# Kernel optimization log

Hardware: AMD Instinct MI355X
Metric: run time of the kernel (lower is better)

Reference implementation:

```python
import jax, jax.numpy as jnp
import numpy as np

# Domain bounds and training nu-range (from init_kwargs)
X_MIN, X_MAX = -1.0, 1.0
Y_MIN, Y_MAX = -1.0, 1.0
T_MIN, T_MAX = 0.0, 1.0
NU_MIN, NU_MAX = 0.01, 0.1

LAYERS = [4, 256, 256, 256, 256, 2]
N = 16384  # collocation points


def setup_inputs() -> dict:
    key = jax.random.key(0)
    ks = jax.random.split(key, 4 + 2 * (len(LAYERS) - 1))
    inp = {
        'x': jax.random.uniform(ks[0], (N, 1), minval=X_MIN, maxval=X_MAX, dtype=jnp.float32),
        'y': jax.random.uniform(ks[1], (N, 1), minval=Y_MIN, maxval=Y_MAX, dtype=jnp.float32),
        't': jax.random.uniform(ks[2], (N, 1), minval=T_MIN, maxval=T_MAX, dtype=jnp.float32),
        'nu': jax.random.uniform(ks[3], (N, 1), minval=NU_MIN, maxval=NU_MAX, dtype=jnp.float32),
    }
    # glorot_normal weights, zero biases (keras Dense defaults)
    for i in range(len(LAYERS) - 1):
        fan_in, fan_out = LAYERS[i], LAYERS[i + 1]
        std = (2.0 / (fan_in + fan_out)) ** 0.5
        inp[f'W{i}'] = std * jax.random.normal(ks[4 + 2 * i], (fan_in, fan_out), dtype=jnp.float32)
        inp[f'b{i}'] = jnp.zeros((fan_out,), dtype=jnp.float32)
    return inp


def _net(pt, nu, params):
    """MLP forward for a single point. pt: (3,) = (x, y, t); nu: scalar. Returns (2,) = (u, v)."""
    x, y, t = pt[0], pt[1], pt[2]
    h = jnp.stack([
        2.0 * (x - X_MIN) / (X_MAX - X_MIN) - 1.0,
        2.0 * (y - Y_MIN) / (Y_MAX - Y_MIN) - 1.0,
        2.0 * (t - T_MIN) / (T_MAX - T_MIN) - 1.0,
        2.0 * (nu - NU_MIN) / (NU_MAX - NU_MIN) - 1.0,
    ])
    for W, b in params[:-1]:
        z = h @ W + b
        h = z * jax.nn.sigmoid(z)  # swish
    W, b = params[-1]
    return h @ W + b


def _residual_point(pt, nu, params):
    """Burgers PDE residual (f_u, f_v) at one collocation point via nested forward-mode AD."""
    f = lambda p: _net(p, nu, params)
    uv = f(pt)                          # (2,)
    J = jax.jacfwd(f)(pt)               # (2,3): d(u,v)/d(x,y,t)
    H = jax.jacfwd(jax.jacfwd(f))(pt)   # (2,3,3)
    u, v = uv[0], uv[1]
    u_x, u_y, u_t = J[0, 0], J[0, 1], J[0, 2]
    v_x, v_y, v_t = J[1, 0], J[1, 1], J[1, 2]
    u_xx, u_yy = H[0, 0, 0], H[0, 1, 1]
    v_xx, v_yy = H[1, 0, 0], H[1, 1, 1]
    f_u = u_t + u * u_x + v * u_y - nu * (u_xx + u_yy)
    f_v = v_t + u * v_x + v * v_y - nu * (v_xx + v_yy)
    return jnp.stack([f_u, f_v])


def reference(x, y, t, nu, W0, b0, W1, b1, W2, b2, W3, b3, W4, b4):
    params = [(W0, b0), (W1, b1), (W2, b2), (W3, b3), (W4, b4)]
    pts = jnp.concatenate([x, y, t], axis=1)  # (N, 3)
    res = jax.vmap(lambda p, n: _residual_point(p, n, params))(pts, nu[:, 0])
    return res  # (N, 2) = [f_u, f_v]
```

## Files before the change

### kernel.cpp

```cpp
#include <hip/hip_runtime.h>

typedef _Float16 f16;
typedef _Float16 v8hf __attribute__((ext_vector_type(8)));
typedef _Float16 v4hf __attribute__((ext_vector_type(4)));
typedef _Float16 v2hf __attribute__((ext_vector_type(2)));
typedef float    v4f  __attribute__((ext_vector_type(4)));

#define NPTS 16384
#define PTS  8
#define NLAYER_ELEMS 65536

__device__ __forceinline__ int swz(int m, int j) {
    return m * 256 + ((((j >> 3) ^ (m & 7)) << 3) | (j & 7));
}

__global__ void pack_weights(const float* __restrict__ W1, const float* __restrict__ W2,
                             const float* __restrict__ W3, f16* __restrict__ bh,
                             f16* __restrict__ bl) {
    const int L = blockIdx.x >> 3, ks = blockIdx.x & 7, n = threadIdx.x;
    const float* W = (L == 0) ? W1 : (L == 1) ? W2 : W3;
    f16 h[32], l[32];
    #pragma unroll
    for (int kk = 0; kk < 32; ++kk) {
        float w = W[(ks * 32 + kk) * 256 + n];
        f16 hh = (f16)w;
        h[kk] = hh;
        l[kk] = (f16)(w - (float)hh);
    }
    size_t off = (size_t)L * NLAYER_ELEMS + (size_t)(ks * 256 + n) * 32;
    #pragma unroll
    for (int i = 0; i < 4; ++i) {
        *(v8hf*)(bh + off + 8 * i) = *(v8hf*)(h + 8 * i);
        *(v8hf*)(bl + off + 8 * i) = *(v8hf*)(l + 8 * i);
    }
}

__global__ __launch_bounds__(256, 3) void pinn_burgers_kernel(
    const float* __restrict__ gx, const float* __restrict__ gy,
    const float* __restrict__ gt, const float* __restrict__ gnu,
    const float* __restrict__ W0, const float* __restrict__ b0,
    const float* __restrict__ b1, const float* __restrict__ b2,
    const float* __restrict__ b3,
    const float* __restrict__ W4, const float* __restrict__ b4,
    const f16* __restrict__ bh, const f16* __restrict__ bl,
    float* __restrict__ out)
{
    __shared__ f16 Ah[48 * 256];
    __shared__ f16 Al[48 * 256];
    __shared__ float red[PTS][12];
    __shared__ float pin[4][PTS];

    const int tid  = threadIdx.x;
    const int lane = tid & 63;
    const int wv   = tid >> 6;
    const int ln   = lane & 15;
    const int quad = lane >> 4;
    const int lnx  = ln & 7;
    const int p0   = blockIdx.x * PTS;

    if (tid < 4 * PTS) {
        int c = tid >> 3, p = tid & 7;
        const float* src = (c == 0) ? gx : (c == 1) ? gy : (c == 2) ? gt : gnu;
        pin[c][p] = src[p0 + p];
    }
    __syncthreads();

    const int l5 = lane & 31;
    const int j0 = wv * 64 + l5 * 2;
    const int ph = (lane >> 5) * 4;

    {
        float w00[2], w01[2], w02[2], w03[2], bb[2];
        #pragma unroll
        for (int e = 0; e < 2; ++e) {
            int j = j0 + e;
            w00[e] = W0[j]; w01[e] = W0[256 + j]; w02[e] = W0[512 + j]; w03[e] = W0[768 + j];
            bb[e] = b0[j];
        }
        #pragma unroll
        for (int pp = 0; pp < 4; ++pp) {
            int p = ph + pp;
            float hx = pin[0][p];
            float hy = pin[1][p];
            float ht = 2.f * pin[2][p] - 1.f;
            float hn = 2.f * (pin[3][p] - 0.01f) * (1.f / 0.09f) - 1.f;
            float a[6][2];
            #pragma unroll
            for (int e = 0; e < 2; ++e) {
                float z  = hx * w00[e] + hy * w01[e] + ht * w02[e] + hn * w03[e] + bb[e];
                float zx = w00[e], zy = w01[e], zt = 2.f * w02[e];
                float s  = 1.f / (1.f + __expf(-z));
                float g1 = s + z * s * (1.f - s);
                float g2 = s * (1.f - s) * (2.f + z * (1.f - 2.f * s));
                a[0][e] = z * s;
                a[1][e] = g1 * zx; a[2][e] = g1 * zy; a[3][e] = g1 * zt;
                a[4][e] = g2 * zx * zx; a[5][e] = g2 * zy * zy;
            }
            #pragma unroll
            for (int c = 0; c < 6; ++c) {
                int idx = swz(c * PTS + p, j0);
                v2hf hh = { (f16)a[c][0], (f16)a[c][1] };
                v2hf ll = { (f16)(a[c][0] - (float)hh[0]), (f16)(a[c][1] - (float)hh[1]) };
                *(v2hf*)&Ah[idx] = hh;
                *(v2hf*)&Al[idx] = ll;
            }
        }
    }
    __syncthreads();

    const float* bias_ptr[3] = { b1, b2, b3 };
    for (int L = 0; L < 3; ++L) {
        const f16* __restrict__ bhL = bh + (size_t)L * NLAYER_ELEMS;
        const f16* __restrict__ blL = bl + (size_t)L * NLAYER_ELEMS;
        const float* __restrict__ bv = bias_ptr[L];

        v4f acc[4][3];
        #pragma unroll
        for (int t = 0; t < 4; ++t)
            #pragma unroll
            for (int mt = 0; mt < 3; ++mt)
                acc[t][mt] = (v4f){0.f, 0.f, 0.f, 0.f};

        #pragma unroll 2
        for (int ks = 0; ks < 8; ++ks) {
            const int cb = (((4 * ks + quad) ^ lnx) << 3);
            v8hf a_h[3], a_l[3];
            #pragma unroll
            for (int mt = 0; mt < 3; ++mt) {
                const int rb = (mt * 16 + ln) * 256 + cb;
                a_h[mt] = *(const v8hf*)&Ah[rb];
                a_l[mt] = *(const v8hf*)&Al[rb];
            }
            v8hf w_h[4], w_l[4];
            #pragma unroll
            for (int t = 0; t < 4; ++t) {
                int n = wv * 64 + t * 16 + ln;
                size_t o = (size_t)(ks * 256 + n) * 32 + quad * 8;
                w_h[t] = *(const v8hf*)(bhL + o);
                w_l[t] = *(const v8hf*)(blL + o);
            }
            #pragma unroll
            for (int t = 0; t < 4; ++t)
                #pragma unroll
                for (int mt = 0; mt < 3; ++mt) {
                    acc[t][mt] = __builtin_amdgcn_mfma_f32_16x16x32_f16(w_h[t], a_h[mt], acc[t][mt], 0, 0, 0);
                    acc[t][mt] = __builtin_amdgcn_mfma_f32_16x16x32_f16(w_h[t], a_l[mt], acc[t][mt], 0, 0, 0);
                    acc[t][mt] = __builtin_amdgcn_mfma_f32_16x16x32_f16(w_l[t], a_h[mt], acc[t][mt], 0, 0, 0);
                }
        }
        __syncthreads();

        #pragma unroll
        for (int t = 0; t < 4; ++t)
            #pragma unroll
            for (int mt = 0; mt < 3; ++mt) {
                v4f a = acc[t][mt];
                int nb = wv * 64 + t * 16 + quad * 4;
                int m  = mt * 16 + ln;
                if (mt == 0 && ln < PTS) {
                    const float4 bq = *(const float4*)(bv + nb);
                    a[0] += bq.x; a[1] += bq.y; a[2] += bq.z; a[3] += bq.w;
                }
                v4hf hi = { (f16)a[0], (f16)a[1], (f16)a[2], (f16)a[3] };
                v4hf lo = { (f16)(a[0] - (float)hi[0]), (f16)(a[1] - (float)hi[1]),
                            (f16)(a[2] - (float)hi[2]), (f16)(a[3] - (float)hi[3]) };
                int idx = swz(m, nb);
                *(v4hf*)&Ah[idx] = hi;
                *(v4hf*)&Al[idx] = lo;
            }

        {
            #pragma unroll
            for (int pp = 0; pp < 4; ++pp) {
                int p = ph + pp;
                float z[6][2];
                #pragma unroll
                for (int c = 0; c < 6; ++c) {
                    int idx = swz(c * PTS + p, j0);
                    v2hf hh = *(v2hf*)&Ah[idx];
                    v2hf ll = *(v2hf*)&Al[idx];
                    z[c][0] = (float)hh[0] + (float)ll[0];
                    z[c][1] = (float)hh[1] + (float)ll[1];
                }
                float a[6][2];
                #pragma unroll
                for (int e = 0; e < 2; ++e) {
                    float zz = z[0][e];
                    float s  = 1.f / (1.f + __expf(-zz));
                    float g1 = s + zz * s * (1.f - s);
                    float g2 = s * (1.f - s) * (2.f + zz * (1.f - 2.f * s));
                    a[0][e] = zz * s;
                    a[1][e] = g1 * z[1][e];
                    a[2][e] = g1 * z[2][e];
                    a[3][e] = g1 * z[3][e];
                    a[4][e] = g2 * z[1][e] * z[1][e] + g1 * z[4][e];
                    a[5][e] = g2 * z[2][e] * z[2][e] + g1 * z[5][e];
                }
                #pragma unroll
                for (int c = 0; c < 6; ++c) {
                    int idx = swz(c * PTS + p, j0);
                    v2hf hh = { (f16)a[c][0], (f16)a[c][1] };
                    v2hf ll = { (f16)(a[c][0] - (float)hh[0]), (f16)(a[c][1] - (float)hh[1]) };
                    *(v2hf*)&Ah[idx] = hh;
                    *(v2hf*)&Al[idx] = ll;
                }
            }
        }
        __syncthreads();
    }

    #pragma unroll
    for (int d = 0; d < 24; ++d) {
        int D  = wv * 24 + d;
        int p  = D / 12;
        int rm = D % 12;
        int c  = rm >> 1;
        int o  = rm & 1;
        int m  = c * PTS + p;
        int k0 = lane * 4;
        int idx = swz(m, k0);
        v4hf hh = *(v4hf*)&Ah[idx];
        v4hf ll = *(v4hf*)&Al[idx];
        float partial = 0.f;
        #pragma unroll
        for (int i = 0; i < 4; ++i)
            partial += ((float)hh[i] + (float)ll[i]) * W4[(k0 + i) * 2 + o];
        #pragma unroll
        for (int off = 32; off > 0; off >>= 1)
            partial += __shfl_down(partial, off);
        if (lane == 0)
            red[p][rm] = partial + ((c == 0) ? b4[o] : 0.f);
    }
    __syncthreads();

    if (tid < PTS) {
        int p = tid;
        float u   = red[p][0],  v   = red[p][1];
        float ux  = red[p][2],  vx  = red[p][3];
        float uy  = red[p][4],  vy  = red[p][5];
        float ut  = red[p][6],  vt  = red[p][7];
        float uxx = red[p][8],  vxx = red[p][9];
        float uyy = red[p][10], vyy = red[p][11];
        float nuv = pin[3][p];
        float fu = ut + u * ux + v * uy - nuv * (uxx + uyy);
        float fv = vt + u * vx + v * vy - nuv * (vxx + vyy);
        out[(p0 + p) * 2 + 0] = fu;
        out[(p0 + p) * 2 + 1] = fv;
    }
}

extern "C" void kernel_launch(void* const* d_in, const int* in_sizes, int n_in,
                              void* d_out, int out_size, void* d_ws, size_t ws_size,
                              hipStream_t stream) {
    const float* x  = (const float*)d_in[0];
    const float* y  = (const float*)d_in[1];
    const float* t  = (const float*)d_in[2];
    const float* nu = (const float*)d_in[3];
    const float* W0 = (const float*)d_in[4];
    const float* b0 = (const float*)d_in[5];
    const float* W1 = (const float*)d_in[6];
    const float* b1 = (const float*)d_in[7];
    const float* W2 = (const float*)d_in[8];
    const float* b2 = (const float*)d_in[9];
    const float* W3 = (const float*)d_in[10];
    const float* b3 = (const float*)d_in[11];
    const float* W4 = (const float*)d_in[12];
    const float* b4 = (const float*)d_in[13];
    float* o = (float*)d_out;

    f16* bh = (f16*)d_ws;
    f16* bl = bh + 3 * (size_t)NLAYER_ELEMS;

    hipLaunchKernelGGL(pack_weights, dim3(24), dim3(256), 0, stream, W1, W2, W3, bh, bl);
    hipLaunchKernelGGL(pinn_burgers_kernel, dim3(NPTS / PTS), dim3(256), 0, stream,
                       x, y, t, nu, W0, b0, b1, b2, b3, W4, b4, bh, bl, o);
}
```

Measured before the change: 221.2 us.

## Fuse swish-derivative epilogue into MFMA accumulator registers via lane shuffles

Applies the swish value, gradient and Hessian transform directly on the MFMA accumulator registers, using a lane xor-shuffle to pair the z value with its derivative rows. This removes the round trip of writing pre-activations to shared memory and reading them back before writing activations. It also switches the fp16 hi/lo splits to packed round-toward-zero conversions, and spreads the weight packing over more blocks with fewer rows per thread. Round-toward-zero changes rounding slightly, though the lo term keeps most of the lost precision.

```diff
diff --git a/kernel.cpp b/kernel.cpp
--- a/kernel.cpp
+++ b/kernel.cpp
@@ -4,12 +4,18 @@
 typedef _Float16 v8hf __attribute__((ext_vector_type(8)));
 typedef _Float16 v4hf __attribute__((ext_vector_type(4)));
 typedef _Float16 v2hf __attribute__((ext_vector_type(2)));
+typedef __fp16   v2pk __attribute__((ext_vector_type(2)));
 typedef float    v4f  __attribute__((ext_vector_type(4)));
 
 #define NPTS 16384
 #define PTS  8
 #define NLAYER_ELEMS 65536
 
+__device__ __forceinline__ v2hf pkrtz(float a, float b) {
+    v2pk r = __builtin_amdgcn_cvt_pkrtz(a, b);
+    return __builtin_bit_cast(v2hf, r);
+}
+
 __device__ __forceinline__ int swz(int m, int j) {
     return m * 256 + ((((j >> 3) ^ (m & 7)) << 3) | (j & 7));
 }
@@ -17,22 +23,37 @@
 __global__ void pack_weights(const float* __restrict__ W1, const float* __restrict__ W2,
                              const float* __restrict__ W3, f16* __restrict__ bh,
                              f16* __restrict__ bl) {
-    const int L = blockIdx.x >> 3, ks = blockIdx.x & 7, n = threadIdx.x;
+    const int b  = blockIdx.x;
+    const int q  = b & 3;
+    const int ks = (b >> 2) & 7;
+    const int L  = b >> 5;
     const float* W = (L == 0) ? W1 : (L == 1) ? W2 : W3;
-    f16 h[32], l[32];
+    const int n   = q * 64 + (threadIdx.x & 63);
+    const int kk0 = (threadIdx.x >> 6) * 8;
+    f16 h[8], l[8];
     #pragma unroll
-    for (int kk = 0; kk < 32; ++kk) {
-        float w = W[(ks * 32 + kk) * 256 + n];
+    for (int i = 0; i < 8; ++i) {
+        float w = W[(ks * 32 + kk0 + i) * 256 + n];
         f16 hh = (f16)w;
-        h[kk] = hh;
-        l[kk] = (f16)(w - (float)hh);
-    }
-    size_t off = (size_t)L * NLAYER_ELEMS + (size_t)(ks * 256 + n) * 32;
-    #pragma unroll
-    for (int i = 0; i < 4; ++i) {
-        *(v8hf*)(bh + off + 8 * i) = *(v8hf*)(h + 8 * i);
-        *(v8hf*)(bl + off + 8 * i) = *(v8hf*)(l + 8 * i);
-    }
+        h[i] = hh;
+        l[i] = (f16)(w - (float)hh);
+    }
+    size_t off = (size_t)L * NLAYER_ELEMS + (size_t)(ks * 256 + n) * 32 + kk0;
+    *(v8hf*)(bh + off) = *(v8hf*)h;
+    *(v8hf*)(bl + off) = *(v8hf*)l;
+}
+
+__device__ __forceinline__ void store_split(const float* a, int m, int nb,
+                                            f16* __restrict__ Ah, f16* __restrict__ Al) {
+    v2hf h01 = pkrtz(a[0], a[1]);
+    v2hf h23 = pkrtz(a[2], a[3]);
+    v2hf l01 = pkrtz(a[0] - (float)h01[0], a[1] - (float)h01[1]);
+    v2hf l23 = pkrtz(a[2] - (float)h23[0], a[3] - (float)h23[1]);
+    v4hf hi = { h01[0], h01[1], h23[0], h23[1] };
+    v4hf lo = { l01[0], l01[1], l23[0], l23[1] };
+    int idx = swz(m, nb);
+    *(v4hf*)&Ah[idx] = hi;
+    *(v4hf*)&Al[idx] = lo;
 }
 
 __global__ __launch_bounds__(256, 3) void pinn_burgers_kernel(
@@ -65,11 +86,10 @@
     }
     __syncthreads();
 
-    const int l5 = lane & 31;
-    const int j0 = wv * 64 + l5 * 2;
-    const int ph = (lane >> 5) * 4;
-
     {
+        const int l5 = lane & 31;
+        const int j0 = wv * 64 + l5 * 2;
+        const int ph = (lane >> 5) * 4;
         float w00[2], w01[2], w02[2], w03[2], bb[2];
         #pragma unroll
         for (int e = 0; e < 2; ++e) {
@@ -99,8 +119,8 @@
             #pragma unroll
             for (int c = 0; c < 6; ++c) {
                 int idx = swz(c * PTS + p, j0);
-                v2hf hh = { (f16)a[c][0], (f16)a[c][1] };
-                v2hf ll = { (f16)(a[c][0] - (float)hh[0]), (f16)(a[c][1] - (float)hh[1]) };
+                v2hf hh = pkrtz(a[c][0], a[c][1]);
+                v2hf ll = pkrtz(a[c][0] - (float)hh[0], a[c][1] - (float)hh[1]);
                 *(v2hf*)&Ah[idx] = hh;
                 *(v2hf*)&Al[idx] = ll;
             }
@@ -150,61 +170,33 @@
         }
         __syncthreads();
 
-        #pragma unroll
-        for (int t = 0; t < 4; ++t)
-            #pragma unroll
-            for (int mt = 0; mt < 3; ++mt) {
-                v4f a = acc[t][mt];
-                int nb = wv * 64 + t * 16 + quad * 4;
-                int m  = mt * 16 + ln;
-                if (mt == 0 && ln < PTS) {
-                    const float4 bq = *(const float4*)(bv + nb);
-                    a[0] += bq.x; a[1] += bq.y; a[2] += bq.z; a[3] += bq.w;
-                }
-                v4hf hi = { (f16)a[0], (f16)a[1], (f16)a[2], (f16)a[3] };
-                v4hf lo = { (f16)(a[0] - (float)hi[0]), (f16)(a[1] - (float)hi[1]),
-                            (f16)(a[2] - (float)hi[2]), (f16)(a[3] - (float)hi[3]) };
-                int idx = swz(m, nb);
-                *(v4hf*)&Ah[idx] = hi;
-                *(v4hf*)&Al[idx] = lo;
-            }
-
-        {
-            #pragma unroll
-            for (int pp = 0; pp < 4; ++pp) {
-                int p = ph + pp;
-                float z[6][2];
-                #pragma unroll
-                for (int c = 0; c < 6; ++c) {
-                    int idx = swz(c * PTS + p, j0);
-                    v2hf hh = *(v2hf*)&Ah[idx];
-                    v2hf ll = *(v2hf*)&Al[idx];
-                    z[c][0] = (float)hh[0] + (float)ll[0];
-                    z[c][1] = (float)hh[1] + (float)ll[1];
-                }
-                float a[6][2];
-                #pragma unroll
-                for (int e = 0; e < 2; ++e) {
-                    float zz = z[0][e];
-                    float s  = 1.f / (1.f + __expf(-zz));
-                    float g1 = s + zz * s * (1.f - s);
-                    float g2 = s * (1.f - s) * (2.f + zz * (1.f - 2.f * s));
-                    a[0][e] = zz * s;
-                    a[1][e] = g1 * z[1][e];
-                    a[2][e] = g1 * z[2][e];
-                    a[3][e] = g1 * z[3][e];
-                    a[4][e] = g2 * z[1][e] * z[1][e] + g1 * z[4][e];
-                    a[5][e] = g2 * z[2][e] * z[2][e] + g1 * z[5][e];
-                }
-                #pragma unroll
-                for (int c = 0; c < 6; ++c) {
-                    int idx = swz(c * PTS + p, j0);
-                    v2hf hh = { (f16)a[c][0], (f16)a[c][1] };
-                    v2hf ll = { (f16)(a[c][0] - (float)hh[0]), (f16)(a[c][1] - (float)hh[1]) };
-                    *(v2hf*)&Ah[idx] = hh;
-                    *(v2hf*)&Al[idx] = ll;
-                }
-            }
+        const bool isA = (ln < 8);
+        #pragma unroll
+        for (int t = 0; t < 4; ++t) {
+            const int nb = wv * 64 + t * 16 + quad * 4;
+            const float4 bq = *(const float4*)(bv + nb);
+            const float bsel[4] = { isA ? bq.x : 0.f, isA ? bq.y : 0.f,
+                                    isA ? bq.z : 0.f, isA ? bq.w : 0.f };
+            float a0v[4], a1v[4], a2v[4];
+            #pragma unroll
+            for (int r = 0; r < 4; ++r) {
+                float accv0 = acc[t][0][r] + bsel[r];
+                float acc1  = acc[t][1][r];
+                float acc2  = acc[t][2][r];
+                float o0 = __shfl_xor(accv0, 8);
+                float o1 = __shfl_xor(acc1, 8);
+                float z  = isA ? accv0 : o0;
+                float sq = isA ? o0    : o1;
+                float s  = 1.f / (1.f + __expf(-z));
+                float g1 = s + z * s * (1.f - s);
+                float g2 = s * (1.f - s) * (2.f + z * (1.f - 2.f * s));
+                a0v[r] = isA ? (z * s) : (g1 * accv0);
+                a1v[r] = g1 * acc1;
+                a2v[r] = g2 * sq * sq + g1 * acc2;
+            }
+            store_split(a0v, ln,      nb, Ah, Al);
+            store_split(a1v, 16 + ln, nb, Ah, Al);
+            store_split(a2v, 32 + ln, nb, Ah, Al);
         }
         __syncthreads();
     }
@@ -271,7 +263,7 @@
     f16* bh = (f16*)d_ws;
     f16* bl = bh + 3 * (size_t)NLAYER_ELEMS;
 
-    hipLaunchKernelGGL(pack_weights, dim3(24), dim3(256), 0, stream, W1, W2, W3, bh, bl);
+    hipLaunchKernelGGL(pack_weights, dim3(96), dim3(256), 0, stream, W1, W2, W3, bh, bl);
     hipLaunchKernelGGL(pinn_burgers_kernel, dim3(NPTS / PTS), dim3(256), 0, stream,
                        x, y, t, nu, W0, b0, b1, b2, b3, W4, b4, bh, bl, o);
 }
```

Measured after the change: 224.5 us. No clear change (+1.5%).
